# Kernel tuning notes

Hardware: AMD Instinct MI355X
Metric: run time of the kernel (lower is better)

Reference implementation:

```python
import jax, jax.numpy as jnp
import numpy as np

N = 100000  # nodes per cluster
E = 1000000  # nonzeros per sparse Laplacian
D = 64       # embedding_size
LEAKY_SLOPE = 0.2  # tf.nn.leaky_relu default alpha


def spmm(rows, cols, vals, dense, num_rows):
    """Sparse [num_rows, M] (COO) @ dense [M, D] -> [num_rows, D]."""
    gathered = vals[:, None] * dense[cols]  # [E, D]
    return jax.ops.segment_sum(gathered, rows, num_segments=num_rows)


def setup_inputs() -> dict:
    key = jax.random.key(0)
    ks = jax.random.split(key, 10)
    return {
        "ebs": jax.random.normal(ks[0], (N, D), dtype=jnp.float32),
        "entity_ebs": jax.random.normal(ks[1], (N, D), dtype=jnp.float32),
        "W_side": jax.random.normal(ks[2], (D, D), dtype=jnp.float32),
        "W_dot": jax.random.normal(ks[3], (D, D), dtype=jnp.float32),
        "LI_vals": jax.random.uniform(ks[4], (E,), dtype=jnp.float32),
        "L_vals": jax.random.uniform(ks[5], (E,), dtype=jnp.float32),
        "LI_rows": jax.random.randint(ks[6], (E,), 0, N, dtype=jnp.int32),
        "LI_cols": jax.random.randint(ks[7], (E,), 0, N, dtype=jnp.int32),
        "L_rows": jax.random.randint(ks[8], (E,), 0, N, dtype=jnp.int32),
        "L_cols": jax.random.randint(ks[9], (E,), 0, N, dtype=jnp.int32),
    }


def reference(ebs, entity_ebs, W_side, W_dot, LI_vals, L_vals,
              LI_rows, LI_cols, L_rows, L_cols) -> jnp.ndarray:
    # __build_weight_graph
    LI_side_embed = spmm(LI_rows, LI_cols, LI_vals, ebs, N)   # [N, D]
    L_side_embed = spmm(L_rows, L_cols, L_vals, ebs, N)       # [N, D]
    sum_embed = LI_side_embed @ W_side                          # [N, D]
    dot_embed = (L_side_embed * entity_ebs) @ W_dot             # [N, D]
    return jax.nn.leaky_relu(sum_embed + dot_embed, negative_slope=LEAKY_SLOPE)
```

## Files before the change

### kernel.cpp

```cpp
#include <hip/hip_runtime.h>

#define D        64
#define BINROWS  64
#define SUBCAP   256
#define NSHARD   8
#define NBINS_MAX 1568
#define CHUNK    3072
#define PER_TH   (CHUNK / 256)
#define FS16     72
#define CURSTRIDE 16

typedef __attribute__((ext_vector_type(8))) short short8;
typedef __attribute__((ext_vector_type(4))) float floatx4;

__device__ __forceinline__ unsigned short f2bf(float f) {
    unsigned u = __float_as_uint(f);
    u += 0x7fffu + ((u >> 16) & 1u);
    return (unsigned short)(u >> 16);
}
__device__ __forceinline__ float bf2f(unsigned short u) {
    return __uint_as_float(((unsigned)u) << 16);
}

__global__ __launch_bounds__(256) void expand_bin_kernel(
    const int* __restrict__ LI_rows, const int* __restrict__ LI_cols, const float* __restrict__ LI_vals,
    const int* __restrict__ L_rows,  const int* __restrict__ L_cols,  const float* __restrict__ L_vals,
    int* __restrict__ cursorP, uint2* __restrict__ seg, int E, int nbins,
    const float* __restrict__ ebs, unsigned short* __restrict__ ebs16, int total4,
    const float* __restrict__ W_side, const float* __restrict__ W_dot,
    unsigned short* __restrict__ Wfrag)
{
    __shared__ uint2 sorted[CHUNK];
    __shared__ unsigned short sbin[CHUNK];
    __shared__ int hist[NBINS_MAX];
    __shared__ int cur[NBINS_MAX];
    __shared__ int gbase[NBINS_MAX];
    __shared__ int tsum[256];

    int t  = threadIdx.x;

    for (int i = blockIdx.x * 256 + t; i < total4; i += gridDim.x * 256) {
        float4 v = ((const float4*)ebs)[i];
        ushort4 o;
        o.x = f2bf(v.x); o.y = f2bf(v.y); o.z = f2bf(v.z); o.w = f2bf(v.w);
        ((ushort4*)ebs16)[i] = o;
    }
    if (blockIdx.x < 4) {
        int tt = blockIdx.x * 256 + t;
        int f = tt >> 6;
        int l = tt & 63;
        int jt = f >> 2, kt = f & 3;
        int q = l >> 4, nl = l & 15;
        int nn = jt * 16 + nl;
#pragma unroll
        for (int j = 0; j < 8; ++j) {
            int k = kt * 32 + q * 8 + j;
            float w = (k < 64) ? W_side[k * 64 + nn] : W_dot[(k - 64) * 64 + nn];
            Wfrag[(size_t)f * 512 + l * 8 + j] = f2bf(w);
        }
    }

    int c0 = blockIdx.x * CHUNK;
    int sh = blockIdx.x & (NSHARD - 1);
    int twoE = 2 * E;
    int chunkcnt = twoE - c0; if (chunkcnt > CHUNK) chunkcnt = CHUNK;

    for (int b = t; b < NBINS_MAX; b += 256) hist[b] = 0;
    __syncthreads();

    unsigned rm[PER_TH];
    uint2    cv[PER_TH];

#pragma unroll
    for (int k = 0; k < PER_TH; ++k) {
        int e = c0 + k * 256 + t;
        rm[k] = 0xFFFFFFFFu;
        if (e < twoE) {
            int m = (e >= E) ? 1 : 0;
            int r, cl; float v;
            if (m) { r = L_rows[e - E]; cl = L_cols[e - E]; v = L_vals[e - E]; }
            else   { r = LI_rows[e];    cl = LI_cols[e];    v = LI_vals[e]; }
            rm[k] = (unsigned)r | ((unsigned)m << 17);
            cv[k] = make_uint2((unsigned)cl, __float_as_uint(v));
            atomicAdd(&hist[r >> 6], 1);
        }
    }
    __syncthreads();

    int loc[7]; int tot = 0;
    if (t < 224) {
#pragma unroll
        for (int i = 0; i < 7; ++i) { loc[i] = tot; tot += hist[t * 7 + i]; }
    }
    tsum[t] = (t < 224) ? tot : 0;
    __syncthreads();
    for (int step = 1; step < 256; step <<= 1) {
        int add = (t >= step) ? tsum[t - step] : 0;
        __syncthreads();
        tsum[t] += add;
        __syncthreads();
    }
    int tbase = tsum[t] - ((t < 224) ? tot : 0);
    if (t < 224) {
#pragma unroll
        for (int i = 0; i < 7; ++i) {
            int key = t * 7 + i;
            cur[key] = tbase + loc[i];
        }
    }
    __syncthreads();

    for (int b = t; b < nbins; b += 256) {
        int c = hist[b];
        gbase[b] = c ? atomicAdd(&cursorP[(sh * NBINS_MAX + b) * CURSTRIDE], c) : 0;
    }

#pragma unroll
    for (int k = 0; k < PER_TH; ++k) {
        unsigned g = rm[k];
        if (g == 0xFFFFFFFFu) continue;
        int r   = (int)(g & 0x1FFFFu);
        int m   = (int)((g >> 17) & 1u);
        int bin = r >> 6;
        int rank = atomicAdd(&cur[bin], 1);
        sorted[rank] = make_uint2(((unsigned)m << 23) | ((unsigned)(r & 63) << 17) | cv[k].x, cv[k].y);
        sbin[rank]   = (unsigned short)bin;
    }
    __syncthreads();

    for (int i = t; i < chunkcnt; i += 256) {
        int bin = sbin[i];
        int off = cur[bin] - hist[bin];
        int pos = gbase[bin] + (i - off);
        if (pos < SUBCAP)
            seg[((size_t)(sh * NBINS_MAX) + bin) * SUBCAP + pos] = sorted[i];
    }
}

__global__ __launch_bounds__(256) void fused_kernel(
    const uint2* __restrict__ seg, const int* __restrict__ cursorP,
    const unsigned short* __restrict__ ebs16,
    const float* __restrict__ entity,
    const unsigned short* __restrict__ Wfrag,
    float* __restrict__ out, int n)
{
    __shared__ __align__(16) char shmem[2 * BINROWS * FS16 * 2];
    __shared__ int hist[128];
    __shared__ int offs[128];
    __shared__ int cur[128];
    uint2* sseg = (uint2*)shmem;
    unsigned short* facc = (unsigned short*)shmem;

    int t = threadIdx.x;
    int b = blockIdx.x;

    if (t < 128) hist[t] = 0;
    __syncthreads();

    int clen[NSHARD];
    uint2 held[NSHARD];
    unsigned hmask = 0;
#pragma unroll
    for (int sh = 0; sh < NSHARD; ++sh) {
        int c = cursorP[(sh * NBINS_MAX + b) * CURSTRIDE];
        clen[sh] = c < SUBCAP ? c : SUBCAP;
        if (t < clen[sh]) {
            held[sh] = seg[((size_t)(sh * NBINS_MAX) + b) * SUBCAP + t];
            hmask |= (1u << sh);
            atomicAdd(&hist[(held[sh].x >> 17) & 127u], 1);
        }
    }
    __syncthreads();

    if (t < 128) offs[t] = hist[t];
    __syncthreads();
    for (int step = 1; step < 128; step <<= 1) {
        int add = 0;
        if (t < 128 && t >= step) add = offs[t - step];
        __syncthreads();
        if (t < 128) offs[t] += add;
        __syncthreads();
    }
    if (t < 128) {
        int excl = offs[t] - hist[t];
        offs[t] = excl;
        cur[t]  = excl;
    }
    __syncthreads();

#pragma unroll
    for (int sh = 0; sh < NSHARD; ++sh) {
        if (hmask & (1u << sh)) {
            unsigned key = (held[sh].x >> 17) & 127u;
            int rank = atomicAdd(&cur[key], 1);
            sseg[rank] = held[sh];
        }
    }
    __syncthreads();

    int g  = t >> 4;
    int l4 = (t & 15) << 2;
    int beg[8], len[8], lenm1[8];
    int maxlen = 0;
#pragma unroll
    for (int kk = 0; kk < 8; ++kk) {
        int key = g * 8 + kk;
        beg[kk]   = offs[key];
        len[kk]   = hist[key];
        lenm1[kk] = len[kk] > 0 ? len[kk] - 1 : 0;
        maxlen = max(maxlen, len[kk]);
    }
    floatx4 a8[8];
#pragma unroll
    for (int kk = 0; kk < 8; ++kk) a8[kk] = (floatx4){0.f, 0.f, 0.f, 0.f};

    for (int s = 0; s < maxlen; ++s) {
#pragma unroll
        for (int kk = 0; kk < 8; ++kk) {
            bool sel = s < len[kk];
            int idx  = beg[kk] + min(s, lenm1[kk]);
            uint2 en = sseg[idx];
            float vv = sel ? __uint_as_float(en.y) : 0.f;
            ushort4 x = *(const ushort4*)(ebs16 + (size_t)(en.x & 0x1FFFFu) * D + l4);
            a8[kk][0] += vv * bf2f(x.x);
            a8[kk][1] += vv * bf2f(x.y);
            a8[kk][2] += vv * bf2f(x.z);
            a8[kk][3] += vv * bf2f(x.w);
        }
    }
    __syncthreads();

#pragma unroll
    for (int kk = 0; kk < 8; ++kk) {
        int key = g * 8 + kk;
        ushort4 o;
        o.x = f2bf(a8[kk][0]); o.y = f2bf(a8[kk][1]);
        o.z = f2bf(a8[kk][2]); o.w = f2bf(a8[kk][3]);
        *(ushort4*)(facc + ((size_t)(key >> 6) * BINROWS + (key & 63)) * FS16 + l4) = o;
    }
    __syncthreads();

    int w = t >> 6;
    int l = t & 63;
    int q = l >> 4, mcol = l & 15;
    int rowbase = b * BINROWS + w * 16;
    int growA = rowbase + mcol;
    int binrow = w * 16 + mcol;
    const unsigned short* faccLI = facc;
    const unsigned short* faccL  = facc + BINROWS * FS16;

    floatx4 accv[4];
#pragma unroll
    for (int jt = 0; jt < 4; ++jt) accv[jt] = (floatx4){0.f, 0.f, 0.f, 0.f};

#pragma unroll
    for (int kt = 0; kt < 4; ++kt) {
        short8 af;
        if (kt < 2) {
            af = *(const short8*)(faccLI + (size_t)binrow * FS16 + kt * 32 + q * 8);
        } else {
            short8 lv = *(const short8*)(faccL + (size_t)binrow * FS16 + (kt - 2) * 32 + q * 8);
            float4 e0 = make_float4(0.f, 0.f, 0.f, 0.f), e1 = e0;
            if (growA < n) {
                const float4* ep = (const float4*)(entity + (size_t)growA * D + (kt - 2) * 32 + q * 8);
                e0 = ep[0]; e1 = ep[1];
            }
            af[0] = (short)f2bf(bf2f((unsigned short)lv[0]) * e0.x);
            af[1] = (short)f2bf(bf2f((unsigned short)lv[1]) * e0.y);
            af[2] = (short)f2bf(bf2f((unsigned short)lv[2]) * e0.z);
            af[3] = (short)f2bf(bf2f((unsigned short)lv[3]) * e0.w);
            af[4] = (short)f2bf(bf2f((unsigned short)lv[4]) * e1.x);
            af[5] = (short)f2bf(bf2f((unsigned short)lv[5]) * e1.y);
            af[6] = (short)f2bf(bf2f((unsigned short)lv[6]) * e1.z);
            af[7] = (short)f2bf(bf2f((unsigned short)lv[7]) * e1.w);
        }
#pragma unroll
        for (int jt = 0; jt < 4; ++jt) {
            const short8 bf = *(const short8*)(Wfrag + (size_t)(jt * 4 + kt) * 512 + (size_t)l * 8);
            accv[jt] = __builtin_amdgcn_mfma_f32_16x16x32_bf16(af, bf, accv[jt], 0, 0, 0);
        }
    }

#pragma unroll
    for (int jt = 0; jt < 4; ++jt) {
#pragma unroll
        for (int r = 0; r < 4; ++r) {
            int grow = rowbase + q * 4 + r;
            if (grow < n) {
                float v = accv[jt][r];
                v = v > 0.f ? v : 0.2f * v;
                out[(size_t)grow * D + jt * 16 + mcol] = v;
            }
        }
    }
}

__global__ void scatter_kernel(
    const float* __restrict__ LI_vals, const int* __restrict__ LI_rows, const int* __restrict__ LI_cols,
    const float* __restrict__ L_vals,  const int* __restrict__ L_rows,  const int* __restrict__ L_cols,
    const float* __restrict__ ebs,
    float* __restrict__ accLI, float* __restrict__ accL, int E)
{
    long long t = (long long)blockIdx.x * blockDim.x + threadIdx.x;
    long long e2 = t >> 4;
    if (e2 >= 2LL * E) return;
    int c = ((int)t & 15) << 2;
    const float* vals; const int* rows; const int* cols; float* acc; int e;
    if (e2 < E) { vals = LI_vals; rows = LI_rows; cols = LI_cols; acc = accLI; e = (int)e2; }
    else        { vals = L_vals;  rows = L_rows;  cols = L_cols;  acc = accL;  e = (int)(e2 - E); }
    float v = vals[e]; int r = rows[e]; int cl = cols[e];
    const float4 x = *(const float4*)(ebs + (size_t)cl * D + c);
    float* o = acc + (size_t)r * D + c;
    unsafeAtomicAdd(o + 0, v * x.x);
    unsafeAtomicAdd(o + 1, v * x.y);
    unsafeAtomicAdd(o + 2, v * x.z);
    unsafeAtomicAdd(o + 3, v * x.w);
}

__global__ __launch_bounds__(256) void epilogue_kernel(
    const float* __restrict__ acc, const float* __restrict__ entity,
    const float* __restrict__ W_side, const float* __restrict__ W_dot,
    float* __restrict__ out, int n)
{
    int lane = threadIdx.x & 63;
    int wave = (blockIdx.x << 2) | (threadIdx.x >> 6);
    int row  = (wave << 6) + lane;
    bool valid = row < n;
    const float* accLI = acc;
    const float* accL  = acc + (size_t)n * D;
    float a[D], b[D];
    if (valid) {
        const float4* ap = (const float4*)(accLI  + (size_t)row * D);
        const float4* lp = (const float4*)(accL   + (size_t)row * D);
        const float4* ep = (const float4*)(entity + (size_t)row * D);
#pragma unroll
        for (int qq = 0; qq < 16; ++qq) {
            float4 av = ap[qq]; float4 lv = lp[qq]; float4 ev = ep[qq];
            a[4*qq+0] = av.x; a[4*qq+1] = av.y; a[4*qq+2] = av.z; a[4*qq+3] = av.w;
            b[4*qq+0] = lv.x * ev.x; b[4*qq+1] = lv.y * ev.y;
            b[4*qq+2] = lv.z * ev.z; b[4*qq+3] = lv.w * ev.w;
        }
    } else {
#pragma unroll
        for (int qq = 0; qq < D; ++qq) { a[qq] = 0.f; b[qq] = 0.f; }
    }
    float4* op = (float4*)(out + (size_t)row * D);
#pragma unroll 1
    for (int jc = 0; jc < 16; ++jc) {
        float a0 = 0.f, a1 = 0.f, a2 = 0.f, a3 = 0.f;
#pragma unroll
        for (int k = 0; k < D; ++k) {
            float4 w1 = *(const float4*)(W_side + (k << 6) + (jc << 2));
            float4 w2 = *(const float4*)(W_dot  + (k << 6) + (jc << 2));
            a0 += a[k] * w1.x + b[k] * w2.x;
            a1 += a[k] * w1.y + b[k] * w2.y;
            a2 += a[k] * w1.z + b[k] * w2.z;
            a3 += a[k] * w1.w + b[k] * w2.w;
        }
        float4 r;
        r.x = a0 > 0.f ? a0 : 0.2f * a0;
        r.y = a1 > 0.f ? a1 : 0.2f * a1;
        r.z = a2 > 0.f ? a2 : 0.2f * a2;
        r.w = a3 > 0.f ? a3 : 0.2f * a3;
        if (valid) op[jc] = r;
    }
}

extern "C" void kernel_launch(void* const* d_in, const int* in_sizes, int n_in,
                              void* d_out, int out_size, void* d_ws, size_t ws_size,
                              hipStream_t stream) {
    const float* ebs     = (const float*)d_in[0];
    const float* entity  = (const float*)d_in[1];
    const float* W_side  = (const float*)d_in[2];
    const float* W_dot   = (const float*)d_in[3];
    const float* LI_vals = (const float*)d_in[4];
    const float* L_vals  = (const float*)d_in[5];
    const int*   LI_rows = (const int*)d_in[6];
    const int*   LI_cols = (const int*)d_in[7];
    const int*   L_rows  = (const int*)d_in[8];
    const int*   L_cols  = (const int*)d_in[9];
    float* out = (float*)d_out;

    int E = in_sizes[4];
    int n = in_sizes[0] / D;
    int nbins = (n + BINROWS - 1) / BINROWS;

    size_t curBytes = (size_t)NSHARD * NBINS_MAX * CURSTRIDE * sizeof(int);
    size_t segBytes = (size_t)NSHARD * NBINS_MAX * SUBCAP * sizeof(uint2);
    size_t ebsBytes = (size_t)n * D * sizeof(unsigned short);
    size_t wfBytes  = (size_t)16 * 512 * sizeof(unsigned short);
    size_t need = curBytes + segBytes + ebsBytes + wfBytes;

    if (ws_size >= need && nbins <= NBINS_MAX && n <= 131072) {
        int*            cursorP = (int*)d_ws;
        uint2*          seg     = (uint2*)((char*)d_ws + curBytes);
        unsigned short* ebs16   = (unsigned short*)((char*)d_ws + curBytes + segBytes);
        unsigned short* Wfrag   = (unsigned short*)((char*)d_ws + curBytes + segBytes + ebsBytes);

        hipMemsetAsync(cursorP, 0, curBytes, stream);

        int total4 = n * D / 4;
        int xblocks = (2 * E + CHUNK - 1) / CHUNK;
        expand_bin_kernel<<<xblocks, 256, 0, stream>>>(
            LI_rows, LI_cols, LI_vals, L_rows, L_cols, L_vals,
            cursorP, seg, E, nbins,
            ebs, ebs16, total4, W_side, W_dot, Wfrag);

        fused_kernel<<<nbins, 256, 0, stream>>>(
            seg, cursorP, ebs16, entity, Wfrag, out, n);
    } else {
        size_t accBytes = (size_t)2 * n * D * sizeof(float);
        float* acc   = (float*)d_ws;
        float* accLI = acc;
        float* accL  = accLI + (size_t)n * D;
        hipMemsetAsync(d_ws, 0, accBytes, stream);
        long long totalThreads = 2LL * E * 16;
        int sblocks = (int)((totalThreads + 255) / 256);
        scatter_kernel<<<sblocks, 256, 0, stream>>>(
            LI_vals, LI_rows, LI_cols, L_vals, L_rows, L_cols, ebs, accLI, accL, E);
        int nTiles = (n + 63) / 64;
        epilogue_kernel<<<(nTiles + 3) / 4, 256, 0, stream>>>(
            acc, entity, W_side, W_dot, out, n);
    }
}
```

Measured before the change: 228.9 us.

## Double fused kernel block size and unroll gather loop by two

Launches the fused SpMM+GEMM kernel with 512 threads per block instead of 256. Each thread now owns 4 row-keys instead of 8, and bin entries are loaded into LDS across 4 slots instead of 8. The gather loop issues loads for two consecutive entries before accumulating, which exposes more memory-level parallelism, and invalid slots point at row 0 instead of a clamped index. Only the first 256 threads run the MFMA epilogue, so half the block sits idle during that phase.

```diff
diff --git a/kernel.cpp b/kernel.cpp
--- a/kernel.cpp
+++ b/kernel.cpp
@@ -9,6 +9,7 @@
 #define PER_TH   (CHUNK / 256)
 #define FS16     72
 #define CURSTRIDE 16
+#define FTH      512
 
 typedef __attribute__((ext_vector_type(8))) short short8;
 typedef __attribute__((ext_vector_type(4))) float floatx4;
@@ -137,7 +138,7 @@
     }
 }
 
-__global__ __launch_bounds__(256) void fused_kernel(
+__global__ __launch_bounds__(FTH) void fused_kernel(
     const uint2* __restrict__ seg, const int* __restrict__ cursorP,
     const unsigned short* __restrict__ ebs16,
     const float* __restrict__ entity,
@@ -158,16 +159,22 @@
     __syncthreads();
 
     int clen[NSHARD];
-    uint2 held[NSHARD];
-    unsigned hmask = 0;
 #pragma unroll
     for (int sh = 0; sh < NSHARD; ++sh) {
         int c = cursorP[(sh * NBINS_MAX + b) * CURSTRIDE];
         clen[sh] = c < SUBCAP ? c : SUBCAP;
-        if (t < clen[sh]) {
-            held[sh] = seg[((size_t)(sh * NBINS_MAX) + b) * SUBCAP + t];
-            hmask |= (1u << sh);
-            atomicAdd(&hist[(held[sh].x >> 17) & 127u], 1);
+    }
+    uint2 held[4];
+    unsigned hmask = 0;
+#pragma unroll
+    for (int k = 0; k < 4; ++k) {
+        int i   = k * FTH + t;
+        int sh  = i >> 8;
+        int pos = i & 255;
+        if (pos < clen[sh]) {
+            held[k] = seg[((size_t)(sh * NBINS_MAX) + b) * SUBCAP + pos];
+            hmask |= (1u << k);
+            atomicAdd(&hist[(held[k].x >> 17) & 127u], 1);
         }
     }
     __syncthreads();
@@ -189,107 +196,136 @@
     __syncthreads();
 
 #pragma unroll
-    for (int sh = 0; sh < NSHARD; ++sh) {
-        if (hmask & (1u << sh)) {
-            unsigned key = (held[sh].x >> 17) & 127u;
+    for (int k = 0; k < 4; ++k) {
+        if (hmask & (1u << k)) {
+            unsigned key = (held[k].x >> 17) & 127u;
             int rank = atomicAdd(&cur[key], 1);
-            sseg[rank] = held[sh];
+            sseg[rank] = held[k];
         }
     }
     __syncthreads();
 
     int g  = t >> 4;
     int l4 = (t & 15) << 2;
-    int beg[8], len[8], lenm1[8];
+    int beg[4], len[4], lenm1[4];
     int maxlen = 0;
 #pragma unroll
-    for (int kk = 0; kk < 8; ++kk) {
-        int key = g * 8 + kk;
+    for (int kk = 0; kk < 4; ++kk) {
+        int key = g * 4 + kk;
         beg[kk]   = offs[key];
         len[kk]   = hist[key];
         lenm1[kk] = len[kk] > 0 ? len[kk] - 1 : 0;
         maxlen = max(maxlen, len[kk]);
     }
-    floatx4 a8[8];
-#pragma unroll
-    for (int kk = 0; kk < 8; ++kk) a8[kk] = (floatx4){0.f, 0.f, 0.f, 0.f};
-
-    for (int s = 0; s < maxlen; ++s) {
-#pragma unroll
-        for (int kk = 0; kk < 8; ++kk) {
+    floatx4 a4[4];
+#pragma unroll
+    for (int kk = 0; kk < 4; ++kk) a4[kk] = (floatx4){0.f, 0.f, 0.f, 0.f};
+
+    for (int s = 0; s < maxlen; s += 2) {
+        float vA[4], vB[4];
+        ushort4 xA[4], xB[4];
+#pragma unroll
+        for (int kk = 0; kk < 4; ++kk) {
             bool sel = s < len[kk];
             int idx  = beg[kk] + min(s, lenm1[kk]);
             uint2 en = sseg[idx];
-            float vv = sel ? __uint_as_float(en.y) : 0.f;
-            ushort4 x = *(const ushort4*)(ebs16 + (size_t)(en.x & 0x1FFFFu) * D + l4);
-            a8[kk][0] += vv * bf2f(x.x);
-            a8[kk][1] += vv * bf2f(x.y);
-            a8[kk][2] += vv * bf2f(x.z);
-            a8[kk][3] += vv * bf2f(x.w);
-        }
-    }
-    __syncthreads();
-
-#pragma unroll
-    for (int kk = 0; kk < 8; ++kk) {
-        int key = g * 8 + kk;
+            vA[kk] = sel ? __uint_as_float(en.y) : 0.f;
+            unsigned enx = sel ? (en.x & 0x1FFFFu) : 0u;
+            xA[kk] = *(const ushort4*)(ebs16 + (enx << 6) + l4);
+        }
+#pragma unroll
+        for (int kk = 0; kk < 4; ++kk) {
+            int s1   = s + 1;
+            bool sel = s1 < len[kk];
+            int idx  = beg[kk] + min(s1, lenm1[kk]);
+            uint2 en = sseg[idx];
+            vB[kk] = sel ? __uint_as_float(en.y) : 0.f;
+            unsigned enx = sel ? (en.x & 0x1FFFFu) : 0u;
+            xB[kk] = *(const ushort4*)(ebs16 + (enx << 6) + l4);
+        }
+#pragma unroll
+        for (int kk = 0; kk < 4; ++kk) {
+            float vv = vA[kk];
+            ushort4 x = xA[kk];
+            a4[kk][0] += vv * bf2f(x.x);
+            a4[kk][1] += vv * bf2f(x.y);
+            a4[kk][2] += vv * bf2f(x.z);
+            a4[kk][3] += vv * bf2f(x.w);
+        }
+#pragma unroll
+        for (int kk = 0; kk < 4; ++kk) {
+            float vv = vB[kk];
+            ushort4 x = xB[kk];
+            a4[kk][0] += vv * bf2f(x.x);
+            a4[kk][1] += vv * bf2f(x.y);
+            a4[kk][2] += vv * bf2f(x.z);
+            a4[kk][3] += vv * bf2f(x.w);
+        }
+    }
+    __syncthreads();
+
+#pragma unroll
+    for (int kk = 0; kk < 4; ++kk) {
+        int key = g * 4 + kk;
         ushort4 o;
-        o.x = f2bf(a8[kk][0]); o.y = f2bf(a8[kk][1]);
-        o.z = f2bf(a8[kk][2]); o.w = f2bf(a8[kk][3]);
+        o.x = f2bf(a4[kk][0]); o.y = f2bf(a4[kk][1]);
+        o.z = f2bf(a4[kk][2]); o.w = f2bf(a4[kk][3]);
         *(ushort4*)(facc + ((size_t)(key >> 6) * BINROWS + (key & 63)) * FS16 + l4) = o;
     }
     __syncthreads();
 
-    int w = t >> 6;
-    int l = t & 63;
-    int q = l >> 4, mcol = l & 15;
-    int rowbase = b * BINROWS + w * 16;
-    int growA = rowbase + mcol;
-    int binrow = w * 16 + mcol;
-    const unsigned short* faccLI = facc;
-    const unsigned short* faccL  = facc + BINROWS * FS16;
-
-    floatx4 accv[4];
-#pragma unroll
-    for (int jt = 0; jt < 4; ++jt) accv[jt] = (floatx4){0.f, 0.f, 0.f, 0.f};
-
-#pragma unroll
-    for (int kt = 0; kt < 4; ++kt) {
-        short8 af;
-        if (kt < 2) {
-            af = *(const short8*)(faccLI + (size_t)binrow * FS16 + kt * 32 + q * 8);
-        } else {
-            short8 lv = *(const short8*)(faccL + (size_t)binrow * FS16 + (kt - 2) * 32 + q * 8);
-            float4 e0 = make_float4(0.f, 0.f, 0.f, 0.f), e1 = e0;
-            if (growA < n) {
-                const float4* ep = (const float4*)(entity + (size_t)growA * D + (kt - 2) * 32 + q * 8);
-                e0 = ep[0]; e1 = ep[1];
+    if (t < 256) {
+        int w = t >> 6;
+        int l = t & 63;
+        int q = l >> 4, mcol = l & 15;
+        int rowbase = b * BINROWS + w * 16;
+        int growA = rowbase + mcol;
+        int binrow = w * 16 + mcol;
+        const unsigned short* faccLI = facc;
+        const unsigned short* faccL  = facc + BINROWS * FS16;
+
+        floatx4 accv[4];
+#pragma unroll
+        for (int jt = 0; jt < 4; ++jt) accv[jt] = (floatx4){0.f, 0.f, 0.f, 0.f};
+
+#pragma unroll
+        for (int kt = 0; kt < 4; ++kt) {
+            short8 af;
+            if (kt < 2) {
+                af = *(const short8*)(faccLI + (size_t)binrow * FS16 + kt * 32 + q * 8);
+            } else {
+                short8 lv = *(const short8*)(faccL + (size_t)binrow * FS16 + (kt - 2) * 32 + q * 8);
+                float4 e0 = make_float4(0.f, 0.f, 0.f, 0.f), e1 = e0;
+                if (growA < n) {
+                    const float4* ep = (const float4*)(entity + (size_t)growA * D + (kt - 2) * 32 + q * 8);
+                    e0 = ep[0]; e1 = ep[1];
+                }
+                af[0] = (short)f2bf(bf2f((unsigned short)lv[0]) * e0.x);
+                af[1] = (short)f2bf(bf2f((unsigned short)lv[1]) * e0.y);
+                af[2] = (short)f2bf(bf2f((unsigned short)lv[2]) * e0.z);
+                af[3] = (short)f2bf(bf2f((unsigned short)lv[3]) * e0.w);
+                af[4] = (short)f2bf(bf2f((unsigned short)lv[4]) * e1.x);
+                af[5] = (short)f2bf(bf2f((unsigned short)lv[5]) * e1.y);
+                af[6] = (short)f2bf(bf2f((unsigned short)lv[6]) * e1.z);
+                af[7] = (short)f2bf(bf2f((unsigned short)lv[7]) * e1.w);
             }
-            af[0] = (short)f2bf(bf2f((unsigned short)lv[0]) * e0.x);
-            af[1] = (short)f2bf(bf2f((unsigned short)lv[1]) * e0.y);
-            af[2] = (short)f2bf(bf2f((unsigned short)lv[2]) * e0.z);
-            af[3] = (short)f2bf(bf2f((unsigned short)lv[3]) * e0.w);
-            af[4] = (short)f2bf(bf2f((unsigned short)lv[4]) * e1.x);
-            af[5] = (short)f2bf(bf2f((unsigned short)lv[5]) * e1.y);
-            af[6] = (short)f2bf(bf2f((unsigned short)lv[6]) * e1.z);
-            af[7] = (short)f2bf(bf2f((unsigned short)lv[7]) * e1.w);
-        }
+#pragma unroll
+            for (int jt = 0; jt < 4; ++jt) {
+                const short8 bf = *(const short8*)(Wfrag + (size_t)(jt * 4 + kt) * 512 + (size_t)l * 8);
+                accv[jt] = __builtin_amdgcn_mfma_f32_16x16x32_bf16(af, bf, accv[jt], 0, 0, 0);
+            }
+        }
+
 #pragma unroll
         for (int jt = 0; jt < 4; ++jt) {
-            const short8 bf = *(const short8*)(Wfrag + (size_t)(jt * 4 + kt) * 512 + (size_t)l * 8);
-            accv[jt] = __builtin_amdgcn_mfma_f32_16x16x32_bf16(af, bf, accv[jt], 0, 0, 0);
-        }
-    }
-
-#pragma unroll
-    for (int jt = 0; jt < 4; ++jt) {
-#pragma unroll
-        for (int r = 0; r < 4; ++r) {
-            int grow = rowbase + q * 4 + r;
-            if (grow < n) {
-                float v = accv[jt][r];
-                v = v > 0.f ? v : 0.2f * v;
-                out[(size_t)grow * D + jt * 16 + mcol] = v;
+#pragma unroll
+            for (int r = 0; r < 4; ++r) {
+                int grow = rowbase + q * 4 + r;
+                if (grow < n) {
+                    float v = accv[jt][r];
+                    v = v > 0.f ? v : 0.2f * v;
+                    out[(size_t)grow * D + jt * 16 + mcol] = v;
+                }
             }
         }
     }
@@ -406,7 +442,7 @@
             cursorP, seg, E, nbins,
             ebs, ebs16, total4, W_side, W_dot, Wfrag);
 
-        fused_kernel<<<nbins, 256, 0, stream>>>(
+        fused_kernel<<<nbins, FTH, 0, stream>>>(
             seg, cursorP, ebs16, entity, Wfrag, out, n);
     } else {
         size_t accBytes = (size_t)2 * n * D * sizeof(float);
```

Measured after the change: 229.5 us. About the same (+0.2%).
